# Performance work log

Hardware: AMD Instinct MI355X
Metric: run time of the kernel (lower is better)

The kernel has to match this reference:

```python
import jax, jax.numpy as jnp
import numpy as np

# Kronecker-sparse patterns (a,b,c,d), rightmost factor first, matching KSLinear.
PATTERNS = ((1, 64, 64, 64), (64, 64, 64, 1))
IN_SIZE = PATTERNS[0][0] * PATTERNS[0][2] * PATTERNS[0][3]   # 4096
OUT_SIZE = PATTERNS[-1][0] * PATTERNS[-1][1] * PATTERNS[-1][3]  # 4096
N_TOKENS = 16384


def setup_inputs() -> dict:
    key = jax.random.key(0)
    kx, k0, k1, kb = jax.random.split(key, 4)
    x = jax.random.normal(kx, (N_TOKENS, IN_SIZE), dtype=jnp.float32)
    # factors stored in native 4D (a,b,c,d) layout, uniform(-1/sqrt(c), 1/sqrt(c))
    a, b, c, d = PATTERNS[0]
    s0 = 1.0 / np.sqrt(c)
    f0 = jax.random.uniform(k0, (a, b, c, d), jnp.float32, -s0, s0)
    a, b, c, d = PATTERNS[1]
    s1 = 1.0 / np.sqrt(c)
    f1 = jax.random.uniform(k1, (a, b, c, d), jnp.float32, -s1, s1)
    bound = 1.0 / np.sqrt(IN_SIZE)
    bias = jax.random.uniform(kb, (OUT_SIZE,), jnp.float32, -bound, bound)
    return {"x": x, "f0": f0, "f1": f1, "bias": bias}


def _ks_apply(x, factor, pattern):
    # Apply one Kronecker-sparse factor with support I_a (x) 1_{b,c} (x) I_d.
    a, b, c, d = pattern
    batch = x.shape[:-1]
    x = x.reshape(*batch, a, c, d)                      # (..., a, c, d)
    y = jnp.einsum('...acd,abcd->...abd', x, factor)    # contract over c
    return y.reshape(*batch, a * b * d)


def reference(x, f0, f1, bias):
    y = _ks_apply(x, f0, PATTERNS[0])
    y = _ks_apply(y, f1, PATTERNS[1])
    return y + bias
```

## Files before the change

### kernel.cpp

```cpp
#include <hip/hip_runtime.h>
#include <cstdint>
#include <cstddef>

#define DI __device__ __forceinline__

using f32x4  = __attribute__((ext_vector_type(4))) float;
using bf16x8 = __attribute__((ext_vector_type(8))) short;
using u32x2  = __attribute__((ext_vector_type(2))) unsigned int;
using u32x4  = __attribute__((ext_vector_type(4))) unsigned int;

constexpr int NT = 16384;
constexpr int NF = 4096;

DI unsigned short f2bf(float f) {
  union { float f; unsigned u; } v; v.f = f;
  unsigned u = v.u;
  u += 0x7fffu + ((u >> 16) & 1u);
  return (unsigned short)(u >> 16);
}

DI void gload_lds16(const void* g, void* l) {
  __builtin_amdgcn_global_load_lds(
      (const __attribute__((address_space(1))) unsigned int*)g,
      (__attribute__((address_space(3))) unsigned int*)l, 16, 0, 0);
}

__global__ void ks_prep(const float* __restrict__ f0, const float* __restrict__ f1,
                        unsigned short* __restrict__ f0s, unsigned short* __restrict__ f1s) {
  int tid = blockIdx.x * 256 + threadIdx.x;
  if (tid < 262144) {
    int d = tid & 63, c = (tid >> 6) & 63, b = tid >> 12;
    f0s[d * 4096 + b * 64 + c] = f2bf(f0[tid]);
  } else {
    int t2 = tid - 262144;
    f1s[t2] = f2bf(f1[t2]);
  }
}

__global__ __launch_bounds__(512, 4) void ks1(
    const float* __restrict__ x, const unsigned short* __restrict__ f0s,
    unsigned short* __restrict__ yp)
{
  __shared__ __align__(16) char L[32768 + 2 * 16640];
  char* const Xb0 = L;
  char* const Xb1 = L + 16384;
  char* const Yb0 = L + 32768;
  char* const Yb1 = L + 32768 + 16640;

  const int w  = blockIdx.x;
  const int tt = (w & 7) | ((w >> 6) << 3);
  const int dg = (w >> 3) & 7;
  const long T0 = (long)tt * 128;

  const int tid = threadIdx.x, lane = tid & 63, wv = tid >> 6;
  const int l15 = lane & 15, lq = lane >> 4;
  const int d = dg * 8 + wv;

  bf16x8 fA[4][2];
  #pragma unroll
  for (int bt = 0; bt < 4; ++bt)
    #pragma unroll
    for (int kh = 0; kh < 2; ++kh)
      fA[bt][kh] = *(const bf16x8*)(f0s + (size_t)d * 4096 + (bt * 16 + l15) * 64 + kh * 32 + lq * 8);

  const int st_t = tid >> 5, st_c0 = (tid >> 1) & 15, st_dq = tid & 1;
  const float* const xrow0 = x + (T0 + st_t) * (long)NF + dg * 8 + st_dq * 4;
  const int wkey = (st_t & 7) << 4;

  f32x4 r0, r1, r2, r3;
  auto issue = [&](int st) {
    const float* p = xrow0 + (long)st * 16 * NF + st_c0 * 4 * 64;
    r0 = *(const f32x4*)(p);
    r1 = *(const f32x4*)(p + 64);
    r2 = *(const f32x4*)(p + 128);
    r3 = *(const f32x4*)(p + 192);
  };
  auto stageX = [&](char* X) {
    #pragma unroll
    for (int e = 0; e < 4; ++e) {
      int p = st_dq * 4 + e;
      unsigned lo = (unsigned)f2bf(r0[e]) | ((unsigned)f2bf(r1[e]) << 16);
      unsigned hi = (unsigned)f2bf(r2[e]) | ((unsigned)f2bf(r3[e]) << 16);
      *(u32x2*)(X + p * 2048 + st_t * 128 + ((st_c0 * 8) ^ wkey)) = u32x2{lo, hi};
    }
  };

  issue(0);
  stageX(Xb0);
  issue(1);
  __syncthreads();

  const int rkey = (l15 & 7) << 4;

  for (int st = 0; st < 8; ++st) {
    char* const Xc = (st & 1) ? Xb1 : Xb0;
    char* const Xn = (st & 1) ? Xb0 : Xb1;
    char* const Yc = (st & 1) ? Yb1 : Yb0;

    const char* Xs = Xc + wv * 2048 + l15 * 128;
    bf16x8 bx0 = *(const bf16x8*)(Xs + ((0  + lq * 16) ^ rkey));
    bf16x8 bx1 = *(const bf16x8*)(Xs + ((64 + lq * 16) ^ rkey));
    f32x4 acc[4];
    #pragma unroll
    for (int bt = 0; bt < 4; ++bt) {
      acc[bt] = __builtin_amdgcn_mfma_f32_16x16x32_bf16(fA[bt][0], bx0, (f32x4){0.f,0.f,0.f,0.f}, 0, 0, 0);
      acc[bt] = __builtin_amdgcn_mfma_f32_16x16x32_bf16(fA[bt][1], bx1, acc[bt], 0, 0, 0);
    }

    {
      char* Yw = Yc + l15 * 1040 + wv * 2;
      #pragma unroll
      for (int bt = 0; bt < 4; ++bt)
        #pragma unroll
        for (int i = 0; i < 4; ++i)
          *(unsigned short*)(Yw + (bt * 16 + lq * 4 + i) * 16) = f2bf(acc[bt][i]);
    }

    stageX(Xn);
    issue(st + 2 <= 7 ? st + 2 : 7);
    __syncthreads();

    {
      const char* Yr = Yc;
      #pragma unroll
      for (int h = 0; h < 2; ++h) {
        int t = (tid >> 6) + h * 8;
        int c16 = tid & 63;
        u32x4 v = *(const u32x4*)(Yr + t * 1040 + c16 * 16);
        *(u32x4*)(yp + (T0 + st * 16 + t) * (size_t)NF + dg * 512 + c16 * 8) = v;
      }
    }
  }
}

__global__ __launch_bounds__(512, 4) void ks2(
    const unsigned short* __restrict__ yp, const unsigned short* __restrict__ f1s,
    const float* __restrict__ bias, float* __restrict__ out)
{
  __shared__ __align__(16) char Yb[2][32768];

  const int bid = blockIdx.x;
  const int ag  = bid & 7;
  const long T0 = (long)(bid >> 3) * 256;

  const int tid = threadIdx.x, lane = tid & 63, wv = tid >> 6;
  const int l15 = lane & 15, lq = lane >> 4;
  const int a = ag * 8 + wv;

  bf16x8 fa[4][2];
  #pragma unroll
  for (int bt = 0; bt < 4; ++bt)
    #pragma unroll
    for (int kh = 0; kh < 2; ++kh)
      fa[bt][kh] = *(const bf16x8*)(f1s + (size_t)a * 4096 + (bt * 16 + l15) * 64 + kh * 32 + lq * 8);
  f32x4 bv[4];
  #pragma unroll
  for (int bt = 0; bt < 4; ++bt)
    bv[bt] = *(const f32x4*)(bias + a * 64 + bt * 16 + lq * 4);

  auto stage = [&](int tile, int buf) {
    #pragma unroll
    for (int i = 0; i < 4; ++i) {
      const int trow = i * 8 + wv;
      const int g = lane ^ (trow & 7);
      const char* src = (const char*)yp + (T0 + (long)tile * 32 + trow) * 8192
                        + ((g >> 3) << 10) + ag * 128 + (g & 7) * 16;
      gload_lds16(src, &Yb[buf][trow * 1024]);
    }
  };

  stage(0, 0);
  asm volatile("s_waitcnt vmcnt(0)" ::: "memory");
  __syncthreads();

  #pragma unroll
  for (int tile = 0; tile < 8; ++tile) {
    if (tile < 7) stage(tile + 1, (tile + 1) & 1);

    const char* Yt = Yb[tile & 1];
    const int sw = wv ^ (l15 & 7);
    #pragma unroll
    for (int tt = 0; tt < 2; ++tt) {
      const char* Yr = Yt + (tt * 16 + l15) * 1024;
      bf16x8 c0 = *(const bf16x8*)(Yr + ((lq * 8 + sw) * 16));
      bf16x8 c1 = *(const bf16x8*)(Yr + (((4 + lq) * 8 + sw) * 16));
      f32x4 acc[4];
      #pragma unroll
      for (int bt = 0; bt < 4; ++bt) {
        acc[bt] = __builtin_amdgcn_mfma_f32_16x16x32_bf16(fa[bt][0], c0, (f32x4){0.f,0.f,0.f,0.f}, 0, 0, 0);
        acc[bt] = __builtin_amdgcn_mfma_f32_16x16x32_bf16(fa[bt][1], c1, acc[bt], 0, 0, 0);
      }
      float* op = out + (T0 + (long)tile * 32 + tt * 16 + l15) * NF + a * 64 + lq * 4;
      #pragma unroll
      for (int bt = 0; bt < 4; ++bt)
        *(f32x4*)(op + bt * 16) = acc[bt] + bv[bt];
    }

    asm volatile("s_waitcnt vmcnt(8)" ::: "memory");
    __syncthreads();
  }
}

__global__ void ks_naive(const float* __restrict__ x, const float* __restrict__ f0,
                         const float* __restrict__ f1, const float* __restrict__ bias,
                         float* __restrict__ out)
{
  __shared__ float xr[4096];
  __shared__ float yr[4096];
  long t = blockIdx.x;
  int tid = threadIdx.x;
  for (int i = tid; i < 4096; i += 256) xr[i] = x[t * 4096 + i];
  __syncthreads();
  for (int i = tid; i < 4096; i += 256) {
    int b = i >> 6, d = i & 63;
    float s = 0.f;
    for (int c = 0; c < 64; ++c) s += xr[c * 64 + d] * f0[(b * 64 + c) * 64 + d];
    yr[i] = s;
  }
  __syncthreads();
  for (int i = tid; i < 4096; i += 256) {
    int a = i >> 6;
    float s = bias[i];
    for (int c = 0; c < 64; ++c) s += yr[a * 64 + c] * f1[(size_t)i * 64 + c];
    out[t * 4096 + i] = s;
  }
}

extern "C" void kernel_launch(void* const* d_in, const int* in_sizes, int n_in,
                              void* d_out, int out_size, void* d_ws, size_t ws_size,
                              hipStream_t stream) {
  const float* x    = (const float*)d_in[0];
  const float* f0   = (const float*)d_in[1];
  const float* f1   = (const float*)d_in[2];
  const float* bias = (const float*)d_in[3];
  float* out = (float*)d_out;

  const size_t ybytes = (size_t)NT * NF * 2;
  const size_t fbytes = (size_t)64 * 64 * 64 * 2;
  if (ws_size >= ybytes + 2 * fbytes) {
    unsigned short* yw  = (unsigned short*)d_ws;
    unsigned short* f0s = yw + (size_t)NT * NF;
    unsigned short* f1s = f0s + 64 * 64 * 64;
    ks_prep<<<2048, 256, 0, stream>>>(f0, f1, f0s, f1s);
    ks1<<<1024, 512, 0, stream>>>(x, f0s, yw);
    ks2<<<512, 512, 0, stream>>>(yw, f1s, bias, out);
  } else {
    ks_naive<<<NT, 256, 0, stream>>>(x, f0, f1, bias, out);
  }
}
```

Measured before the change: 206.9 us.

## Deepen ks2 LDS pipeline to four 16-row buffers and double grid size

The second-stage kernel now stages 16-token tiles into a 4-deep ring of LDS buffers with three tiles in flight, and waits on explicit vmcnt counts that account for the interleaved output stores. Each block handles 128 tokens instead of 256, so the grid doubles to 1024 blocks for better occupancy and load balance. The aim is to hide global-to-LDS load latency behind the MFMA work and stores. In exchange, the hand-tuned vmcnt values are fragile, and each block has to reload its factor and bias registers for half as many tokens.

```diff
diff --git a/kernel.cpp b/kernel.cpp
--- a/kernel.cpp
+++ b/kernel.cpp
@@ -24,6 +24,13 @@
       (const __attribute__((address_space(1))) unsigned int*)g,
       (__attribute__((address_space(3))) unsigned int*)l, 16, 0, 0);
 }
+
+#define BAR_VM(N)                                              \
+  do {                                                         \
+    asm volatile("s_waitcnt vmcnt(" #N ")" ::: "memory");      \
+    __builtin_amdgcn_s_barrier();                              \
+    __builtin_amdgcn_sched_barrier(0);                         \
+  } while (0)
 
 __global__ void ks_prep(const float* __restrict__ f0, const float* __restrict__ f1,
                         unsigned short* __restrict__ f0s, unsigned short* __restrict__ f1s) {
@@ -137,11 +144,11 @@
     const unsigned short* __restrict__ yp, const unsigned short* __restrict__ f1s,
     const float* __restrict__ bias, float* __restrict__ out)
 {
-  __shared__ __align__(16) char Yb[2][32768];
+  __shared__ __align__(16) char Yb[4][16384];
 
   const int bid = blockIdx.x;
   const int ag  = bid & 7;
-  const long T0 = (long)(bid >> 3) * 256;
+  const long T0 = (long)(bid >> 3) * 128;
 
   const int tid = threadIdx.x, lane = tid & 63, wv = tid >> 6;
   const int l15 = lane & 15, lq = lane >> 4;
@@ -158,46 +165,50 @@
   for (int bt = 0; bt < 4; ++bt)
     bv[bt] = *(const f32x4*)(bias + a * 64 + bt * 16 + lq * 4);
 
-  auto stage = [&](int tile, int buf) {
-    #pragma unroll
-    for (int i = 0; i < 4; ++i) {
+  auto stage = [&](int tile) {
+    char* const dst = Yb[tile & 3];
+    #pragma unroll
+    for (int i = 0; i < 2; ++i) {
       const int trow = i * 8 + wv;
       const int g = lane ^ (trow & 7);
-      const char* src = (const char*)yp + (T0 + (long)tile * 32 + trow) * 8192
+      const char* src = (const char*)yp + (T0 + (long)tile * 16 + trow) * 8192
                         + ((g >> 3) << 10) + ag * 128 + (g & 7) * 16;
-      gload_lds16(src, &Yb[buf][trow * 1024]);
+      gload_lds16(src, dst + trow * 1024);
     }
   };
 
-  stage(0, 0);
-  asm volatile("s_waitcnt vmcnt(0)" ::: "memory");
-  __syncthreads();
-
-  #pragma unroll
-  for (int tile = 0; tile < 8; ++tile) {
-    if (tile < 7) stage(tile + 1, (tile + 1) & 1);
-
-    const char* Yt = Yb[tile & 1];
+  stage(0); stage(1); stage(2);
+  BAR_VM(4);
+
+  #pragma unroll
+  for (int j = 0; j < 8; ++j) {
+    if (j + 3 < 8) stage(j + 3);
+
+    const char* Yr = Yb[j & 3] + l15 * 1024;
     const int sw = wv ^ (l15 & 7);
-    #pragma unroll
-    for (int tt = 0; tt < 2; ++tt) {
-      const char* Yr = Yt + (tt * 16 + l15) * 1024;
-      bf16x8 c0 = *(const bf16x8*)(Yr + ((lq * 8 + sw) * 16));
-      bf16x8 c1 = *(const bf16x8*)(Yr + (((4 + lq) * 8 + sw) * 16));
-      f32x4 acc[4];
-      #pragma unroll
-      for (int bt = 0; bt < 4; ++bt) {
-        acc[bt] = __builtin_amdgcn_mfma_f32_16x16x32_bf16(fa[bt][0], c0, (f32x4){0.f,0.f,0.f,0.f}, 0, 0, 0);
-        acc[bt] = __builtin_amdgcn_mfma_f32_16x16x32_bf16(fa[bt][1], c1, acc[bt], 0, 0, 0);
-      }
-      float* op = out + (T0 + (long)tile * 32 + tt * 16 + l15) * NF + a * 64 + lq * 4;
-      #pragma unroll
-      for (int bt = 0; bt < 4; ++bt)
-        *(f32x4*)(op + bt * 16) = acc[bt] + bv[bt];
-    }
-
-    asm volatile("s_waitcnt vmcnt(8)" ::: "memory");
-    __syncthreads();
+    bf16x8 c0 = *(const bf16x8*)(Yr + ((lq * 8 + sw) * 16));
+    bf16x8 c1 = *(const bf16x8*)(Yr + (((4 + lq) * 8 + sw) * 16));
+    f32x4 acc[4];
+    #pragma unroll
+    for (int bt = 0; bt < 4; ++bt) {
+      acc[bt] = __builtin_amdgcn_mfma_f32_16x16x32_bf16(fa[bt][0], c0, (f32x4){0.f,0.f,0.f,0.f}, 0, 0, 0);
+      acc[bt] = __builtin_amdgcn_mfma_f32_16x16x32_bf16(fa[bt][1], c1, acc[bt], 0, 0, 0);
+    }
+    float* op = out + (T0 + (long)j * 16 + l15) * NF + a * 64 + lq * 4;
+    #pragma unroll
+    for (int bt = 0; bt < 4; ++bt)
+      *(f32x4*)(op + bt * 16) = acc[bt] + bv[bt];
+
+    switch (j) {
+      case 0: BAR_VM(8);  break;
+      case 1: BAR_VM(12); break;
+      case 2: BAR_VM(16); break;
+      case 3: BAR_VM(16); break;
+      case 4: BAR_VM(16); break;
+      case 5: BAR_VM(14); break;
+      case 6: BAR_VM(12); break;
+      default: break;
+    }
   }
 }
 
@@ -243,7 +254,7 @@
     unsigned short* f1s = f0s + 64 * 64 * 64;
     ks_prep<<<2048, 256, 0, stream>>>(f0, f1, f0s, f1s);
     ks1<<<1024, 512, 0, stream>>>(x, f0s, yw);
-    ks2<<<512, 512, 0, stream>>>(yw, f1s, bias, out);
+    ks2<<<1024, 512, 0, stream>>>(yw, f1s, bias, out);
   } else {
     ks_naive<<<NT, 256, 0, stream>>>(x, f0, f1, bias, out);
   }
```

New measurement: 201.8 us. -2.5%, faster.
